# Performance work log

Measured on AMD Instinct MI355X. Metric: run time of the kernel, lower is better.

## Reference

```python
import jax, jax.numpy as jnp
import numpy as np

B, T, E, H = 8, 1024, 768, 12  # batch, num_tokens, embed_dim (=dk=dv), num_heads


def setup_inputs() -> dict:
    key = jax.random.key(0)
    ks = jax.random.split(key, 5)
    return {
        "x": jax.random.normal(ks[0], (B, T, E), dtype=jnp.float32),
        "WQ": jax.random.normal(ks[1], (H, E, E), dtype=jnp.float32),
        "WK": jax.random.normal(ks[2], (H, E, E), dtype=jnp.float32),
        "WV": jax.random.normal(ks[3], (H, E, E), dtype=jnp.float32),
        "WO": jax.random.normal(ks[4], (H * E, E), dtype=jnp.float32),
    }


def reference(x, WQ, WK, WV, WO):
    b, t, e = x.shape
    h = WQ.shape[0]
    dk = WQ.shape[2]
    dv = WV.shape[2]
    # Batched QKV projections for all heads at once: (h, b, t, d)
    Q = jnp.einsum('bte,hek->hbtk', x, WQ)
    K = jnp.einsum('bte,hek->hbtk', x, WK)
    V = jnp.einsum('bte,hev->hbtv', x, WV)
    # Faithful quirk: original does K.view(b, e, t) -- a row-major RESHAPE,
    # not a transpose (valid because dk == e).
    K_rs = K.reshape(h, b, e, t)
    scores = jnp.matmul(Q, K_rs)  # (h, b, t, t)
    # Faithful quirks: scale by sqrt(num_tokens) (K.size(1) == t), and
    # Softmax(1) normalizes over the QUERY axis (axis 1 of (b,t,t) -> axis -2).
    A = jax.nn.softmax(scores / jnp.sqrt(jnp.asarray(t, scores.dtype)), axis=-2)
    Z = jnp.matmul(A, V)  # (h, b, t, dv)
    # Original: Z[bb] has layout (h, t, dv); reshape(t, h*dv) flat in row-major.
    Zc = jnp.transpose(Z, (1, 0, 2, 3)).reshape(b, h, t, dv)
    Zc = Zc.reshape(b, h * t * dv).reshape(b, t, h * dv)  # row-major flat of (h,t,dv)
    return jnp.matmul(Zc, WO)  # (b, t, e)
```

## Files before the change

### kernel.cpp

```cpp
#include <hip/hip_runtime.h>


typedef __bf16 bf16x8 __attribute__((ext_vector_type(8)));
typedef float  f32x4  __attribute__((ext_vector_type(4)));
typedef unsigned short u16;
typedef u16 u16x8 __attribute__((ext_vector_type(8)));
typedef u16 u16x4 __attribute__((ext_vector_type(4)));
typedef unsigned int u32;

#define RC 16

__device__ __forceinline__ float bf2f(u16 u) {
    union { u32 i; float f; } x; x.i = ((u32)u) << 16; return x.f;
}
__device__ __forceinline__ u16 f2bf(float f) {
    __bf16 h = (__bf16)f; union { __bf16 b; u16 u; } x; x.b = h; return x.u;
}
__device__ __forceinline__ void split2(float v, u16& h, u16& l) {
    h = f2bf(v); l = f2bf(v - bf2f(h));
}

__device__ __forceinline__ void gl16(const void* g, void* l) {
    __builtin_amdgcn_global_load_lds(
        (const __attribute__((address_space(1))) u32*)g,
        (__attribute__((address_space(3))) u32*)l, 16, 0, 0);
}

template<int BKMAJ, int WIN>
__device__ __forceinline__ void core(
    const u16* __restrict__ Ah, const u16* __restrict__ Al,
    const u16* __restrict__ Bh, const u16* __restrict__ Bl,
    float* __restrict__ C, u16* __restrict__ Ch, u16* __restrict__ Cl,
    int K, int lda, int ldb, int ldc,
    long long aShift, long long aHi, const u16* __restrict__ zp,
    int mClip, int mode, int mtile, int kChunk, int kChunks, int n0)
{
    __shared__ u16 Ahs[4096], Als[4096], Bhs[4096], Bls[4096];

    const int tid = threadIdx.x, lane = tid & 63, w = tid >> 6;
    const int m0 = mtile * 128;
    const int wm = (w & 1) << 6, wn = (w >> 1) << 6;
    const int lr = lane & 15, lq = lane >> 4;
    const int rs = (lr >> 1) & 3;
    const int fro = (lq ^ rs) << 4;

    const int srow = (w << 4) + (lane >> 2);
    const int kk = (((lane & 3) ^ ((srow >> 1) & 3)) << 3);
    const int lds0 = (w << 10), lds1 = lds0 + 4096;

    const int nB = tid & 127, khB = (tid >> 7) << 4;
    const int rsB = (nB >> 1) & 3;
    const int sB0 = (((khB >> 3) ^ rsB) << 4);
    const int sB1 = ((((khB >> 3) | 1) ^ rsB) << 4);

    f32x4 acc[4][4] = {};
    const int kLen = K / kChunks;
    const int kBeg = kChunk * kLen, kEnd = kBeg + kLen;

    u16 rBh[16], rBl[16];
    auto loadB = [&](int k0) {
        if constexpr (BKMAJ) {
#pragma unroll
            for (int j = 0; j < 16; ++j) {
                long long o = (long long)(k0 + khB + j) * ldb + n0 + nB;
                rBh[j] = Bh[o]; rBl[j] = Bl[o];
            }
        }
    };
    auto stage = [&](int k0) {
        long long o1 = (long long)(m0 + srow) * lda + k0 + kk;
        long long o2 = o1 + (long long)64 * lda;
        const u16 *p1h = Ah + o1, *p1l = Al + o1;
        const u16 *p2h = Ah + o2, *p2l = Al + o2;
        if constexpr (WIN) {
            long long a1 = o1 + aShift, a2 = o2 + aShift;
            bool v1 = (a1 >= 0) && (a1 < aHi);
            bool v2 = (a2 >= 0) && (a2 < aHi);
            p1h = v1 ? Ah + a1 : zp;  p1l = v1 ? Al + a1 : zp;
            p2h = v2 ? Ah + a2 : zp;  p2l = v2 ? Al + a2 : zp;
        }
        gl16(p1h, (char*)Ahs + lds0);  gl16(p2h, (char*)Ahs + lds1);
        gl16(p1l, (char*)Als + lds0);  gl16(p2l, (char*)Als + lds1);
        if constexpr (!BKMAJ) {
            long long b1 = (long long)(n0 + srow) * ldb + k0 + kk;
            long long b2 = b1 + (long long)64 * ldb;
            gl16(Bh + b1, (char*)Bhs + lds0);  gl16(Bh + b2, (char*)Bhs + lds1);
            gl16(Bl + b1, (char*)Bls + lds0);  gl16(Bl + b2, (char*)Bls + lds1);
        }
    };
    auto writeB = [&]() {
        if constexpr (BKMAJ) {
            u16x8 h0, h1, l0, l1;
#pragma unroll
            for (int j = 0; j < 8; ++j) {
                h0[j] = rBh[j]; h1[j] = rBh[j + 8];
                l0[j] = rBl[j]; l1[j] = rBl[j + 8];
            }
            *(u16x8*)((char*)Bhs + nB * 64 + sB0) = h0;
            *(u16x8*)((char*)Bhs + nB * 64 + sB1) = h1;
            *(u16x8*)((char*)Bls + nB * 64 + sB0) = l0;
            *(u16x8*)((char*)Bls + nB * 64 + sB1) = l1;
        }
    };

    loadB(kBeg);
    for (int k0 = kBeg; k0 < kEnd; k0 += 32) {
        stage(k0);
        writeB();
        __syncthreads();
        if (k0 + 32 < kEnd) loadB(k0 + 32);

        bf16x8 a_h[4], a_l[4];
#pragma unroll
        for (int mi = 0; mi < 4; ++mi) {
            int off = ((wm + (mi << 4) + lr) << 6) + fro;
            a_h[mi] = *(const bf16x8*)((char*)Ahs + off);
            a_l[mi] = *(const bf16x8*)((char*)Als + off);
        }
#pragma unroll
        for (int ni = 0; ni < 4; ++ni) {
            int off = ((wn + (ni << 4) + lr) << 6) + fro;
            bf16x8 b_h = *(const bf16x8*)((char*)Bhs + off);
            bf16x8 b_l = *(const bf16x8*)((char*)Bls + off);
#pragma unroll
            for (int mi = 0; mi < 4; ++mi) {
                acc[mi][ni] = __builtin_amdgcn_mfma_f32_16x16x32_bf16(a_h[mi], b_h, acc[mi][ni], 0, 0, 0);
                acc[mi][ni] = __builtin_amdgcn_mfma_f32_16x16x32_bf16(a_l[mi], b_h, acc[mi][ni], 0, 0, 0);
                acc[mi][ni] = __builtin_amdgcn_mfma_f32_16x16x32_bf16(a_h[mi], b_l, acc[mi][ni], 0, 0, 0);
            }
        }
        __syncthreads();
    }

#pragma unroll
    for (int mi = 0; mi < 4; ++mi)
#pragma unroll
        for (int r = 0; r < 4; ++r) {
            int row = m0 + wm + (mi << 4) + (lq << 2) + r;
            if (row < mClip) {
#pragma unroll
                for (int ni = 0; ni < 4; ++ni) {
                    long long off = (long long)row * ldc + n0 + wn + (ni << 4) + lr;
                    float v = acc[mi][ni][r];
                    if (mode == 2)      atomicAdd(&C[off], v);
                    else if (mode == 1) { u16 hh, ll; split2(v, hh, ll); Ch[off] = hh; Cl[off] = ll; }
                    else                C[off] = v;
                }
            }
        }
}

__global__ __launch_bounds__(256, 3)
void g_qkv(const u16* __restrict__ Xh, const u16* __restrict__ Xl,
           const u16* __restrict__ Wth, const u16* __restrict__ Wtl,
           u16* __restrict__ Qh, u16* __restrict__ Ql,
           u16* __restrict__ Kh, u16* __restrict__ Kl,
           u16* __restrict__ Vh, u16* __restrict__ Vl)
{
    const long long EE = 768LL * 768;
    int z = blockIdx.z;
    const u16* bh = Wth + (long long)z * EE;
    const u16* bl = Wtl + (long long)z * EE;
    u16* ch = (z == 0) ? Qh : (z == 1) ? Kh : Vh;
    u16* cl = (z == 0) ? Ql : (z == 1) ? Kl : Vl;
    core<0, 0>(Xh, Xl, bh, bl, nullptr, ch, cl, 768, 768, 768, 768,
               0, 0, nullptr, 1 << 30, 1, blockIdx.y, 0, 1, blockIdx.x * 128);
}

__global__ __launch_bounds__(256, 3)
void g_km(const u16* __restrict__ Ah, const u16* __restrict__ Al,
          const u16* __restrict__ Bh, const u16* __restrict__ Bl,
          u16* __restrict__ Ch, u16* __restrict__ Cl,
          int K, int lda, int ldb, int ldc,
          long long sA, long long sB, long long sC)
{
    long long z = blockIdx.z;
    core<1, 0>(Ah + z * sA, Al + z * sA, Bh + z * sB, Bl + z * sB,
               nullptr, Ch + z * sC, Cl + z * sC,
               K, lda, ldb, ldc, 0, 0, nullptr, 1 << 30, 1,
               blockIdx.y, 0, 1, blockIdx.x * 128);
}

__global__ __launch_bounds__(256, 3)
void g_fin(const u16* __restrict__ Zh, const u16* __restrict__ Zl,
           const u16* __restrict__ WOth, const u16* __restrict__ WOtl,
           float* __restrict__ C, const u16* __restrict__ zp,
           long long aShift, int mClip, int kChunks)
{
    const long long TE_ = 786432;
    long long z = blockIdx.z;
    core<0, 1>(Zh + z * TE_, Zl + z * TE_, WOth, WOtl, C + z * TE_,
               nullptr, nullptr, 9216, 9216, 9216, 768,
               aShift, TE_, zp, mClip, 2, 0, blockIdx.y, kChunks, blockIdx.x * 128);
}

__global__ void k_split(const float* __restrict__ s, u16* __restrict__ h,
                        u16* __restrict__ l, long long n)
{
    long long i = ((long long)blockIdx.x * blockDim.x + threadIdx.x) * 4;
    long long stride = (long long)gridDim.x * blockDim.x * 4;
    for (; i < n; i += stride) {
        float4 v = *(const float4*)(s + i);
        u16x4 hh, ll;
        u16 h0, l0, h1, l1, h2, l2, h3, l3;
        split2(v.x, h0, l0); split2(v.y, h1, l1);
        split2(v.z, h2, l2); split2(v.w, h3, l3);
        hh[0] = h0; hh[1] = h1; hh[2] = h2; hh[3] = h3;
        ll[0] = l0; ll[1] = l1; ll[2] = l2; ll[3] = l3;
        *(u16x4*)(h + i) = hh;
        *(u16x4*)(l + i) = ll;
    }
}

__global__ void k_tsplit(const float* __restrict__ s, u16* __restrict__ dh,
                         u16* __restrict__ dl, int Ks, int Ns)
{
    __shared__ float t[32][33];
    int tx = threadIdx.x & 31, ty = threadIdx.x >> 5;
    int kb = blockIdx.y << 5, nb_ = blockIdx.x << 5;
#pragma unroll
    for (int i = 0; i < 4; ++i)
        t[ty + 8 * i][tx] = s[(long long)(kb + ty + 8 * i) * Ns + nb_ + tx];
    __syncthreads();
#pragma unroll
    for (int i = 0; i < 4; ++i) {
        float v = t[tx][ty + 8 * i];
        long long o = (long long)(nb_ + ty + 8 * i) * Ks + kb + tx;
        u16 hh, ll; split2(v, hh, ll);
        dh[o] = hh; dl[o] = ll;
    }
}

__global__ void k_tsplit3(const float* __restrict__ s0, const float* __restrict__ s1,
                          const float* __restrict__ s2,
                          u16* __restrict__ dh, u16* __restrict__ dl)
{
    const int E = 768; const long long EE = (long long)E * E;
    const float* s = (blockIdx.z == 0) ? s0 : (blockIdx.z == 1) ? s1 : s2;
    u16* h = dh + blockIdx.z * EE;
    u16* l = dl + blockIdx.z * EE;
    __shared__ float t[32][33];
    int tx = threadIdx.x & 31, ty = threadIdx.x >> 5;
    int kb = blockIdx.y << 5, nb_ = blockIdx.x << 5;
#pragma unroll
    for (int i = 0; i < 4; ++i)
        t[ty + 8 * i][tx] = s[(long long)(kb + ty + 8 * i) * E + nb_ + tx];
    __syncthreads();
#pragma unroll
    for (int i = 0; i < 4; ++i) {
        float v = t[tx][ty + 8 * i];
        long long o = (long long)(nb_ + ty + 8 * i) * E + kb + tx;
        u16 hh, ll; split2(v, hh, ll);
        h[o] = hh; l[o] = ll;
    }
}

__global__ __launch_bounds__(256)
void sm_part(const u16* __restrict__ Sh, const u16* __restrict__ Sl,
             float2* __restrict__ part, int T, float scale)
{
    const int lane = threadIdx.x & 63, seg = threadIdx.x >> 6;
    const int j0 = blockIdx.x * 256 + lane * 4;
    const long long base = (long long)blockIdx.z * T * T;
    const int rpc = T / RC, rps = rpc / 4;
    const int r0 = blockIdx.y * rpc + seg * rps;

    float m[4] = {-3.4e38f, -3.4e38f, -3.4e38f, -3.4e38f};
    float s[4] = {0.f, 0.f, 0.f, 0.f};
    for (int r = 0; r < rps; ++r) {
        long long o = base + (long long)(r0 + r) * T + j0;
        u16x4 vh = *(const u16x4*)(Sh + o);
        u16x4 vl = *(const u16x4*)(Sl + o);
#pragma unroll
        for (int c = 0; c < 4; ++c) {
            float v = (bf2f(vh[c]) + bf2f(vl[c])) * scale;
            float mn = fmaxf(m[c], v);
            s[c] = s[c] * __expf(m[c] - mn) + __expf(v - mn);
            m[c] = mn;
        }
    }
    __shared__ float4 smm[4][64], sss[4][64];
    smm[seg][lane] = make_float4(m[0], m[1], m[2], m[3]);
    sss[seg][lane] = make_float4(s[0], s[1], s[2], s[3]);
    __syncthreads();
    if (seg == 0) {
#pragma unroll
        for (int q = 1; q < 4; ++q) {
            float4 mq4 = smm[q][lane], sq4 = sss[q][lane];
            float mq[4] = {mq4.x, mq4.y, mq4.z, mq4.w};
            float sq[4] = {sq4.x, sq4.y, sq4.z, sq4.w};
#pragma unroll
            for (int c = 0; c < 4; ++c) {
                float mn = fmaxf(m[c], mq[c]);
                s[c] = s[c] * __expf(m[c] - mn) + sq[c] * __expf(mq[c] - mn);
                m[c] = mn;
            }
        }
        long long pb = ((long long)blockIdx.z * RC + blockIdx.y) * T + j0;
#pragma unroll
        for (int c = 0; c < 4; ++c)
            part[pb + c] = make_float2(m[c], s[c]);
    }
}

__global__ __launch_bounds__(256)
void sm_fin2(const float2* __restrict__ part, float2* __restrict__ fin, int T)
{
    int j = blockIdx.x * 256 + threadIdx.x;
    long long pb = (long long)blockIdx.y * RC * T + j;
    float mt = -3.4e38f, st = 0.f;
#pragma unroll
    for (int q = 0; q < RC; ++q) {
        float2 p = part[pb + (long long)q * T];
        float mn = fmaxf(mt, p.x);
        st = st * __expf(mt - mn) + p.y * __expf(p.x - mn);
        mt = mn;
    }
    fin[(long long)blockIdx.y * T + j] = make_float2(mt, 1.f / st);
}

__global__ __launch_bounds__(256)
void sm_norm(u16* __restrict__ Sh, u16* __restrict__ Sl,
             const float2* __restrict__ fin, int T, float scale)
{
    const int lane = threadIdx.x & 63, seg = threadIdx.x >> 6;
    const int j0 = blockIdx.x * 256 + lane * 4;
    const long long base = (long long)blockIdx.z * T * T;
    const int rpc = T / RC, rps = rpc / 4;
    const int r0 = blockIdx.y * rpc + seg * rps;
    float mt[4], inv[4];
#pragma unroll
    for (int c = 0; c < 4; ++c) {
        float2 f = fin[(long long)blockIdx.z * T + j0 + c];
        mt[c] = f.x; inv[c] = f.y;
    }
    for (int r = 0; r < rps; ++r) {
        long long o = base + (long long)(r0 + r) * T + j0;
        u16x4 vh = *(const u16x4*)(Sh + o);
        u16x4 vl = *(const u16x4*)(Sl + o);
        u16x4 oh, ol;
#pragma unroll
        for (int c = 0; c < 4; ++c) {
            float v = (bf2f(vh[c]) + bf2f(vl[c])) * scale;
            float p = __expf(v - mt[c]) * inv[c];
            u16 hh, ll; split2(p, hh, ll);
            oh[c] = hh; ol[c] = ll;
        }
        *(u16x4*)(Sh + o) = oh;
        *(u16x4*)(Sl + o) = ol;
    }
}

extern "C" void kernel_launch(void* const* d_in, const int* in_sizes, int n_in,
                              void* d_out, int out_size, void* d_ws, size_t ws_size,
                              hipStream_t stream)
{
    const float* x  = (const float*)d_in[0];
    const float* WQ = (const float*)d_in[1];
    const float* WK = (const float*)d_in[2];
    const float* WV = (const float*)d_in[3];
    const float* WO = (const float*)d_in[4];
    float* out = (float*)d_out;

    const int B = 8, T = 1024, E = 768, H = 12;
    const long long TE = (long long)T * E;
    const long long TT = (long long)T * T;
    const long long HE = (long long)H * E;
    const long long EE = (long long)E * E;

    char* p = (char*)d_ws;
    u16* Xh   = (u16*)p; p += (size_t)B * TE * 2;
    u16* Xl   = (u16*)p; p += (size_t)B * TE * 2;
    u16* WOth = (u16*)p; p += (size_t)E * HE * 2;
    u16* WOtl = (u16*)p; p += (size_t)E * HE * 2;
    u16* Wth  = (u16*)p; p += (size_t)3 * EE * 2;
    u16* Wtl  = (u16*)p; p += (size_t)3 * EE * 2;
    u16* zp   = (u16*)p; p += 4096;
    float2* part = (float2*)p; p += (size_t)B * RC * T * sizeof(float2);
    float2* finb = (float2*)p; p += (size_t)B * T * sizeof(float2);
    size_t used = (size_t)(p - (char*)d_ws);
    size_t slice = (size_t)(6 * TE + 2 * TT) * 2;
    int NC = (int)((ws_size - used) / slice);
    if (NC < 1) NC = 1;
    if (NC > B) NC = B;
    u16* Qh = (u16*)p; p += (size_t)NC * TE * 2;
    u16* Ql = (u16*)p; p += (size_t)NC * TE * 2;
    u16* Kh = (u16*)p; p += (size_t)NC * TE * 2;
    u16* Kl = (u16*)p; p += (size_t)NC * TE * 2;
    u16* Vh = (u16*)p; p += (size_t)NC * TE * 2;
    u16* Vl = (u16*)p; p += (size_t)NC * TE * 2;
    u16* Sh = (u16*)p; p += (size_t)NC * TT * 2;
    u16* Sl = (u16*)p; p += (size_t)NC * TT * 2;
    u16* Zh = Qh;
    u16* Zl = Ql;

    hipMemsetAsync(out, 0, (size_t)B * TE * sizeof(float), stream);
    hipMemsetAsync(zp, 0, 4096, stream);

    dim3 blk(256);

    k_split<<<2048, blk, 0, stream>>>(x, Xh, Xl, (long long)B * TE);
    k_tsplit<<<dim3(E / 32, (int)HE / 32), blk, 0, stream>>>(WO, WOth, WOtl, (int)HE, E);

    for (int h = 0; h < H; ++h) {
        const int i_lo = (int)(((long long)h * TE) / HE);
        const long long aShift = (long long)i_lo * HE - (long long)h * TE;

        k_tsplit3<<<dim3(24, 24, 3), blk, 0, stream>>>(
            WQ + (size_t)h * EE, WK + (size_t)h * EE, WV + (size_t)h * EE, Wth, Wtl);

        for (int b0 = 0; b0 < B; b0 += NC) {
            const int nb = (B - b0 < NC) ? (B - b0) : NC;

            g_qkv<<<dim3(6, nb * T / 128, 3), blk, 0, stream>>>(
                Xh + (size_t)b0 * TE, Xl + (size_t)b0 * TE, Wth, Wtl,
                Qh, Ql, Kh, Kl, Vh, Vl);

            g_km<<<dim3(8, 8, nb), blk, 0, stream>>>(
                Qh, Ql, Kh, Kl, Sh, Sl, 768, 768, 1024, 1024, TE, TE, TT);

            sm_part<<<dim3(T / 256, RC, nb), blk, 0, stream>>>(Sh, Sl, part, T, 0.03125f);
            sm_fin2<<<dim3(T / 256, nb), blk, 0, stream>>>(part, finb, T);
            sm_norm<<<dim3(T / 256, RC, nb), blk, 0, stream>>>(Sh, Sl, finb, T, 0.03125f);

            g_km<<<dim3(6, 8, nb), blk, 0, stream>>>(
                Sh, Sl, Vh, Vl, Zh, Zl, 1024, 1024, 768, 768, TT, TE, TE);

            g_fin<<<dim3(6, 24, nb), blk, 0, stream>>>(
                Zh, Zl, WOth, WOtl,
                out + (size_t)b0 * TE + (size_t)i_lo * E, zp,
                aShift, T - i_lo, 24);
        }
    }
}
```

Measured before the change: 4.289 ms.

## Fuse softmax partials into score GEMM, pre-split all weights, and batch the output projection

Computes the column-wise softmax max/sum partials in the epilogue of the QK^T GEMM, which removes the sm_part and sm_fin2 kernels. sm_norm now merges the partials itself. All heads' QKV weights are transposed and split once up front when the workspace allows it. In the top tier, Z for all heads is stored and a single split-K output projection runs per batch chunk, replacing the per-head g_fin calls. It also loops batch-outer/head-inner, merges the QKV grid into 18 x-blocks, and raises launch bounds to 4 waves per SIMD, which adds register pressure and needs a larger workspace.

```diff
diff --git a/kernel.cpp b/kernel.cpp
--- a/kernel.cpp
+++ b/kernel.cpp
@@ -33,7 +33,8 @@
     float* __restrict__ C, u16* __restrict__ Ch, u16* __restrict__ Cl,
     int K, int lda, int ldb, int ldc,
     long long aShift, long long aHi, const u16* __restrict__ zp,
-    int mClip, int mode, int mtile, int kChunk, int kChunks, int n0)
+    int mClip, int mode, int mtile, int kChunk, int kChunks, int n0,
+    float2* __restrict__ part, float pscale, int pz)
 {
     __shared__ u16 Ahs[4096], Als[4096], Bhs[4096], Bls[4096];
 
@@ -143,14 +144,45 @@
                     long long off = (long long)row * ldc + n0 + wn + (ni << 4) + lr;
                     float v = acc[mi][ni][r];
                     if (mode == 2)      atomicAdd(&C[off], v);
-                    else if (mode == 1) { u16 hh, ll; split2(v, hh, ll); Ch[off] = hh; Cl[off] = ll; }
-                    else                C[off] = v;
+                    else if (mode == 0) C[off] = v;
+                    else { u16 hh, ll; split2(v, hh, ll); Ch[off] = hh; Cl[off] = ll; }
                 }
             }
         }
-}
-
-__global__ __launch_bounds__(256, 3)
+
+    if (mode == 3) {
+#pragma unroll
+        for (int ni = 0; ni < 4; ++ni) {
+            float mloc = -3.4e38f;
+#pragma unroll
+            for (int mi = 0; mi < 4; ++mi)
+#pragma unroll
+                for (int r = 0; r < 4; ++r)
+                    mloc = fmaxf(mloc, acc[mi][ni][r] * pscale);
+            float sl = 0.f;
+#pragma unroll
+            for (int mi = 0; mi < 4; ++mi)
+#pragma unroll
+                for (int r = 0; r < 4; ++r)
+                    sl += __expf(acc[mi][ni][r] * pscale - mloc);
+#pragma unroll
+            for (int off = 16; off < 64; off <<= 1) {
+                float mo = __shfl_xor(mloc, off);
+                float so = __shfl_xor(sl, off);
+                float mn = fmaxf(mloc, mo);
+                sl = sl * __expf(mloc - mn) + so * __expf(mo - mn);
+                mloc = mn;
+            }
+            if (lq == 0) {
+                int j = n0 + wn + (ni << 4) + lr;
+                part[((long long)pz * RC + (mtile << 1) + (wm >> 6)) * 1024 + j]
+                    = make_float2(mloc, sl);
+            }
+        }
+    }
+}
+
+__global__ __launch_bounds__(256, 4)
 void g_qkv(const u16* __restrict__ Xh, const u16* __restrict__ Xl,
            const u16* __restrict__ Wth, const u16* __restrict__ Wtl,
            u16* __restrict__ Qh, u16* __restrict__ Ql,
@@ -158,30 +190,48 @@
            u16* __restrict__ Vh, u16* __restrict__ Vl)
 {
     const long long EE = 768LL * 768;
-    int z = blockIdx.z;
+    int z  = blockIdx.x % 3;
+    int n0 = (blockIdx.x / 3) * 128;
     const u16* bh = Wth + (long long)z * EE;
     const u16* bl = Wtl + (long long)z * EE;
     u16* ch = (z == 0) ? Qh : (z == 1) ? Kh : Vh;
     u16* cl = (z == 0) ? Ql : (z == 1) ? Kl : Vl;
     core<0, 0>(Xh, Xl, bh, bl, nullptr, ch, cl, 768, 768, 768, 768,
-               0, 0, nullptr, 1 << 30, 1, blockIdx.y, 0, 1, blockIdx.x * 128);
-}
-
-__global__ __launch_bounds__(256, 3)
+               0, 0, nullptr, 1 << 30, 1, blockIdx.y, 0, 1, n0,
+               nullptr, 0.f, 0);
+}
+
+__global__ __launch_bounds__(256, 4)
 void g_km(const u16* __restrict__ Ah, const u16* __restrict__ Al,
           const u16* __restrict__ Bh, const u16* __restrict__ Bl,
           u16* __restrict__ Ch, u16* __restrict__ Cl,
           int K, int lda, int ldb, int ldc,
-          long long sA, long long sB, long long sC)
+          long long sA, long long sB, long long sC,
+          float2* part, float pscale, int mode)
 {
     long long z = blockIdx.z;
     core<1, 0>(Ah + z * sA, Al + z * sA, Bh + z * sB, Bl + z * sB,
                nullptr, Ch + z * sC, Cl + z * sC,
-               K, lda, ldb, ldc, 0, 0, nullptr, 1 << 30, 1,
-               blockIdx.y, 0, 1, blockIdx.x * 128);
-}
-
-__global__ __launch_bounds__(256, 3)
+               K, lda, ldb, ldc, 0, 0, nullptr, 1 << 30, mode,
+               blockIdx.y, 0, 1, blockIdx.x * 128, part, pscale, (int)z);
+}
+
+__global__ __launch_bounds__(256, 4)
+void g_out(const u16* __restrict__ Zh, const u16* __restrict__ Zl,
+           const u16* __restrict__ WOth, const u16* __restrict__ WOtl,
+           float* __restrict__ C, int kChunks)
+{
+    const long long ZB = 12LL * 786432;
+    long long z = blockIdx.z;
+    int mtile = blockIdx.y / kChunks;
+    int kc    = blockIdx.y % kChunks;
+    core<0, 0>(Zh + z * ZB, Zl + z * ZB, WOth, WOtl, C + z * 786432LL,
+               nullptr, nullptr, 9216, 9216, 9216, 768,
+               0, 0, nullptr, 1 << 30, 2, mtile, kc, kChunks, blockIdx.x * 128,
+               nullptr, 0.f, 0);
+}
+
+__global__ __launch_bounds__(256, 4)
 void g_fin(const u16* __restrict__ Zh, const u16* __restrict__ Zl,
            const u16* __restrict__ WOth, const u16* __restrict__ WOtl,
            float* __restrict__ C, const u16* __restrict__ zp,
@@ -191,7 +241,8 @@
     long long z = blockIdx.z;
     core<0, 1>(Zh + z * TE_, Zl + z * TE_, WOth, WOtl, C + z * TE_,
                nullptr, nullptr, 9216, 9216, 9216, 768,
-               aShift, TE_, zp, mClip, 2, 0, blockIdx.y, kChunks, blockIdx.x * 128);
+               aShift, TE_, zp, mClip, 2, 0, blockIdx.y, kChunks, blockIdx.x * 128,
+               nullptr, 0.f, 0);
 }
 
 __global__ void k_split(const float* __restrict__ s, u16* __restrict__ h,
@@ -255,73 +306,34 @@
     }
 }
 
-__global__ __launch_bounds__(256)
-void sm_part(const u16* __restrict__ Sh, const u16* __restrict__ Sl,
-             float2* __restrict__ part, int T, float scale)
-{
-    const int lane = threadIdx.x & 63, seg = threadIdx.x >> 6;
-    const int j0 = blockIdx.x * 256 + lane * 4;
-    const long long base = (long long)blockIdx.z * T * T;
-    const int rpc = T / RC, rps = rpc / 4;
-    const int r0 = blockIdx.y * rpc + seg * rps;
-
-    float m[4] = {-3.4e38f, -3.4e38f, -3.4e38f, -3.4e38f};
-    float s[4] = {0.f, 0.f, 0.f, 0.f};
-    for (int r = 0; r < rps; ++r) {
-        long long o = base + (long long)(r0 + r) * T + j0;
-        u16x4 vh = *(const u16x4*)(Sh + o);
-        u16x4 vl = *(const u16x4*)(Sl + o);
-#pragma unroll
-        for (int c = 0; c < 4; ++c) {
-            float v = (bf2f(vh[c]) + bf2f(vl[c])) * scale;
-            float mn = fmaxf(m[c], v);
-            s[c] = s[c] * __expf(m[c] - mn) + __expf(v - mn);
-            m[c] = mn;
-        }
-    }
-    __shared__ float4 smm[4][64], sss[4][64];
-    smm[seg][lane] = make_float4(m[0], m[1], m[2], m[3]);
-    sss[seg][lane] = make_float4(s[0], s[1], s[2], s[3]);
+__global__ void k_tsplitA(const float* __restrict__ WQ, const float* __restrict__ WK,
+                          const float* __restrict__ WV,
+                          u16* __restrict__ dh, u16* __restrict__ dl)
+{
+    const int E = 768; const long long EE = (long long)E * E;
+    int hz = blockIdx.z, hh_ = hz / 3, w = hz % 3;
+    const float* s = ((w == 0) ? WQ : (w == 1) ? WK : WV) + (long long)hh_ * EE;
+    u16* h = dh + (long long)hz * EE;
+    u16* l = dl + (long long)hz * EE;
+    __shared__ float t[32][33];
+    int tx = threadIdx.x & 31, ty = threadIdx.x >> 5;
+    int kb = blockIdx.y << 5, nb_ = blockIdx.x << 5;
+#pragma unroll
+    for (int i = 0; i < 4; ++i)
+        t[ty + 8 * i][tx] = s[(long long)(kb + ty + 8 * i) * E + nb_ + tx];
     __syncthreads();
-    if (seg == 0) {
-#pragma unroll
-        for (int q = 1; q < 4; ++q) {
-            float4 mq4 = smm[q][lane], sq4 = sss[q][lane];
-            float mq[4] = {mq4.x, mq4.y, mq4.z, mq4.w};
-            float sq[4] = {sq4.x, sq4.y, sq4.z, sq4.w};
-#pragma unroll
-            for (int c = 0; c < 4; ++c) {
-                float mn = fmaxf(m[c], mq[c]);
-                s[c] = s[c] * __expf(m[c] - mn) + sq[c] * __expf(mq[c] - mn);
-                m[c] = mn;
-            }
-        }
-        long long pb = ((long long)blockIdx.z * RC + blockIdx.y) * T + j0;
-#pragma unroll
-        for (int c = 0; c < 4; ++c)
-            part[pb + c] = make_float2(m[c], s[c]);
-    }
-}
-
-__global__ __launch_bounds__(256)
-void sm_fin2(const float2* __restrict__ part, float2* __restrict__ fin, int T)
-{
-    int j = blockIdx.x * 256 + threadIdx.x;
-    long long pb = (long long)blockIdx.y * RC * T + j;
-    float mt = -3.4e38f, st = 0.f;
-#pragma unroll
-    for (int q = 0; q < RC; ++q) {
-        float2 p = part[pb + (long long)q * T];
-        float mn = fmaxf(mt, p.x);
-        st = st * __expf(mt - mn) + p.y * __expf(p.x - mn);
-        mt = mn;
-    }
-    fin[(long long)blockIdx.y * T + j] = make_float2(mt, 1.f / st);
+#pragma unroll
+    for (int i = 0; i < 4; ++i) {
+        float v = t[tx][ty + 8 * i];
+        long long o = (long long)(nb_ + ty + 8 * i) * E + kb + tx;
+        u16 hh, ll; split2(v, hh, ll);
+        h[o] = hh; l[o] = ll;
+    }
 }
 
 __global__ __launch_bounds__(256)
 void sm_norm(u16* __restrict__ Sh, u16* __restrict__ Sl,
-             const float2* __restrict__ fin, int T, float scale)
+             const float2* __restrict__ part, int T, float scale)
 {
     const int lane = threadIdx.x & 63, seg = threadIdx.x >> 6;
     const int j0 = blockIdx.x * 256 + lane * 4;
@@ -331,8 +343,15 @@
     float mt[4], inv[4];
 #pragma unroll
     for (int c = 0; c < 4; ++c) {
-        float2 f = fin[(long long)blockIdx.z * T + j0 + c];
-        mt[c] = f.x; inv[c] = f.y;
+        float m = -3.4e38f, s = 0.f;
+#pragma unroll
+        for (int q = 0; q < RC; ++q) {
+            float2 p = part[((long long)blockIdx.z * RC + q) * 1024 + j0 + c];
+            float mn = fmaxf(m, p.x);
+            s = s * __expf(m - mn) + p.y * __expf(p.x - mn);
+            m = mn;
+        }
+        mt[c] = m; inv[c] = 1.f / s;
     }
     for (int r = 0; r < rps; ++r) {
         long long o = base + (long long)(r0 + r) * T + j0;
@@ -373,16 +392,26 @@
     u16* Xl   = (u16*)p; p += (size_t)B * TE * 2;
     u16* WOth = (u16*)p; p += (size_t)E * HE * 2;
     u16* WOtl = (u16*)p; p += (size_t)E * HE * 2;
-    u16* Wth  = (u16*)p; p += (size_t)3 * EE * 2;
-    u16* Wtl  = (u16*)p; p += (size_t)3 * EE * 2;
     u16* zp   = (u16*)p; p += 4096;
     float2* part = (float2*)p; p += (size_t)B * RC * T * sizeof(float2);
-    float2* finb = (float2*)p; p += (size_t)B * T * sizeof(float2);
-    size_t used = (size_t)(p - (char*)d_ws);
-    size_t slice = (size_t)(6 * TE + 2 * TT) * 2;
-    int NC = (int)((ws_size - used) / slice);
-    if (NC < 1) NC = 1;
-    if (NC > B) NC = B;
+    size_t used0 = (size_t)(p - (char*)d_ws);
+
+    const size_t slice = (size_t)(6 * TE + 2 * TT) * 2;
+    const size_t zsl   = (size_t)12 * TE * 4;
+    const size_t wt12  = (size_t)36 * EE * 2 * 2;
+    const size_t wt1   = (size_t)3 * EE * 2 * 2;
+
+    long long avail = (long long)ws_size - (long long)used0;
+    bool wtAll = false, tierA = false;
+    int NC;
+    if (avail >= (long long)(wt12 + 8 * (slice + zsl)))      { wtAll = true; tierA = true; NC = 8; }
+    else if (avail >= (long long)(wt12 + 8 * slice))         { wtAll = true; NC = 8; }
+    else if (avail >= (long long)(wt1 + 8 * slice))          { NC = 8; }
+    else { NC = (int)((avail - (long long)wt1) / (long long)slice); if (NC < 1) NC = 1; }
+
+    u16* Wth = (u16*)p;  u16* Wtl;
+    if (wtAll) { Wtl = Wth + (size_t)36 * EE; p += wt12; }
+    else       { Wtl = Wth + (size_t)3 * EE;  p += wt1;  }
     u16* Qh = (u16*)p; p += (size_t)NC * TE * 2;
     u16* Ql = (u16*)p; p += (size_t)NC * TE * 2;
     u16* Kh = (u16*)p; p += (size_t)NC * TE * 2;
@@ -391,6 +420,8 @@
     u16* Vl = (u16*)p; p += (size_t)NC * TE * 2;
     u16* Sh = (u16*)p; p += (size_t)NC * TT * 2;
     u16* Sl = (u16*)p; p += (size_t)NC * TT * 2;
+    u16* Zallh = (u16*)p; if (tierA) p += (size_t)NC * 12 * TE * 2;
+    u16* Zalll = (u16*)p;
     u16* Zh = Qh;
     u16* Zl = Ql;
 
@@ -401,35 +432,55 @@
 
     k_split<<<2048, blk, 0, stream>>>(x, Xh, Xl, (long long)B * TE);
     k_tsplit<<<dim3(E / 32, (int)HE / 32), blk, 0, stream>>>(WO, WOth, WOtl, (int)HE, E);
-
-    for (int h = 0; h < H; ++h) {
-        const int i_lo = (int)(((long long)h * TE) / HE);
-        const long long aShift = (long long)i_lo * HE - (long long)h * TE;
-
-        k_tsplit3<<<dim3(24, 24, 3), blk, 0, stream>>>(
-            WQ + (size_t)h * EE, WK + (size_t)h * EE, WV + (size_t)h * EE, Wth, Wtl);
-
-        for (int b0 = 0; b0 < B; b0 += NC) {
-            const int nb = (B - b0 < NC) ? (B - b0) : NC;
-
-            g_qkv<<<dim3(6, nb * T / 128, 3), blk, 0, stream>>>(
-                Xh + (size_t)b0 * TE, Xl + (size_t)b0 * TE, Wth, Wtl,
+    if (wtAll)
+        k_tsplitA<<<dim3(24, 24, 36), blk, 0, stream>>>(WQ, WK, WV, Wth, Wtl);
+
+    for (int b0 = 0; b0 < B; b0 += NC) {
+        const int nb = (B - b0 < NC) ? (B - b0) : NC;
+
+        for (int h = 0; h < H; ++h) {
+            const u16* wh; const u16* wl;
+            if (wtAll) { wh = Wth + (size_t)h * 3 * EE; wl = Wtl + (size_t)h * 3 * EE; }
+            else {
+                k_tsplit3<<<dim3(24, 24, 3), blk, 0, stream>>>(
+                    WQ + (size_t)h * EE, WK + (size_t)h * EE, WV + (size_t)h * EE,
+                    Wth, Wtl);
+                wh = Wth; wl = Wtl;
+            }
+
+            g_qkv<<<dim3(18, nb * T / 128), blk, 0, stream>>>(
+                Xh + (size_t)b0 * TE, Xl + (size_t)b0 * TE, wh, wl,
                 Qh, Ql, Kh, Kl, Vh, Vl);
 
             g_km<<<dim3(8, 8, nb), blk, 0, stream>>>(
-                Qh, Ql, Kh, Kl, Sh, Sl, 768, 768, 1024, 1024, TE, TE, TT);
-
-            sm_part<<<dim3(T / 256, RC, nb), blk, 0, stream>>>(Sh, Sl, part, T, 0.03125f);
-            sm_fin2<<<dim3(T / 256, nb), blk, 0, stream>>>(part, finb, T);
-            sm_norm<<<dim3(T / 256, RC, nb), blk, 0, stream>>>(Sh, Sl, finb, T, 0.03125f);
-
-            g_km<<<dim3(6, 8, nb), blk, 0, stream>>>(
-                Sh, Sl, Vh, Vl, Zh, Zl, 1024, 1024, 768, 768, TT, TE, TE);
-
-            g_fin<<<dim3(6, 24, nb), blk, 0, stream>>>(
-                Zh, Zl, WOth, WOtl,
-                out + (size_t)b0 * TE + (size_t)i_lo * E, zp,
-                aShift, T - i_lo, 24);
-        }
-    }
-}
+                Qh, Ql, Kh, Kl, Sh, Sl, 768, 768, 1024, 1024, TE, TE, TT,
+                part, 0.03125f, 3);
+
+            sm_norm<<<dim3(T / 256, RC, nb), blk, 0, stream>>>(
+                Sh, Sl, part, T, 0.03125f);
+
+            if (tierA) {
+                g_km<<<dim3(6, 8, nb), blk, 0, stream>>>(
+                    Sh, Sl, Vh, Vl,
+                    Zallh + (size_t)h * TE, Zalll + (size_t)h * TE,
+                    1024, 1024, 768, 768, TT, TE, 12 * TE,
+                    nullptr, 0.f, 1);
+            } else {
+                const int i_lo = (int)(((long long)h * TE) / HE);
+                const long long aShift = (long long)i_lo * HE - (long long)h * TE;
+                g_km<<<dim3(6, 8, nb), blk, 0, stream>>>(
+                    Sh, Sl, Vh, Vl, Zh, Zl, 1024, 1024, 768, 768, TT, TE, TE,
+                    nullptr, 0.f, 1);
+                g_fin<<<dim3(6, 12, nb), blk, 0, stream>>>(
+                    Zh, Zl, WOth, WOtl,
+                    out + (size_t)b0 * TE + (size_t)i_lo * E, zp,
+                    aShift, T - i_lo, 12);
+            }
+        }
+
+        if (tierA) {
+            g_out<<<dim3(6, 8 * 4, nb), blk, 0, stream>>>(
+                Zallh, Zalll, WOth, WOtl, out + (size_t)b0 * TE, 4);
+        }
+    }
+}
```

Measured after the change: 8.434 ms. +96.6%, slower.
